# Kernel optimization log

Hardware: AMD Instinct MI355X
Metric: run time of the kernel (lower is better)

The kernel has to match this reference:

```python
import jax, jax.numpy as jnp
import numpy as np
from jax import lax

V, D, M, H, NC, S = 100000, 512, 512, 256, 5, 1024


def setup_inputs() -> dict:
    key = jax.random.key(0)
    ks = jax.random.split(key, 16)
    s = 0.05
    emb = jax.random.normal(ks[0], (V, D), jnp.float32) * s
    emb = emb.at[0].set(0.0)  # padding_idx = 0
    inp = {
        "l_ids": jax.random.randint(ks[1], (S,), 0, V),
        "r_ids": jax.random.randint(ks[2], (S,), 0, V),
        "emb": emb,
        "Wioux": jax.random.normal(ks[3], (3 * M, D), jnp.float32) * s,
        "bioux": jnp.zeros((3 * M,), jnp.float32),
        "Wiouh": jax.random.normal(ks[4], (3 * M, M), jnp.float32) * s,
        "biouh": jnp.zeros((3 * M,), jnp.float32),
        "Wfx": jax.random.normal(ks[5], (M, D), jnp.float32) * s,
        "bfx": jnp.zeros((M,), jnp.float32),
        "Wfh": jax.random.normal(ks[6], (M, M), jnp.float32) * s,
        "bfh": jnp.zeros((M,), jnp.float32),
        "Wh": jax.random.normal(ks[7], (H, 4 * M), jnp.float32) * s,
        "bh": jnp.zeros((H,), jnp.float32),
        "Wp": jax.random.normal(ks[8], (NC, H), jnp.float32) * s,
        "bp": jnp.zeros((NC,), jnp.float32),
    }
    return inp


def reference(l_ids, r_ids, emb, Wioux, bioux, Wiouh, biouh, Wfx, bfx, Wfh, bfh, Wh, bh, Wp, bp):
    def cell(x, c, h):
        # i, o, u gates fused into one [3M] GEMV pair, as in the original ioux/iouh Linears
        iou = Wioux @ x + bioux + Wiouh @ h + biouh
        i, o, u = jnp.split(iou, 3)
        f = jax.nn.sigmoid(Wfx @ x + bfx + Wfh @ h + bfh)
        # torch.sum(f*c, dim=0) over a [1, M] tensor is identity -> c' = i*u + f*c
        c2 = jax.nn.sigmoid(i) * jnp.tanh(u) + f * c
        h2 = jax.nn.sigmoid(o) * jnp.tanh(c2)
        return c2, h2

    def encode(xs):  # xs: [S, D]
        z = jnp.zeros((M,), xs.dtype)
        (_, hF), _ = lax.scan(lambda ch, x: (cell(x, ch[0], ch[1]), None), (z, z), xs)
        # 'backward' direction in the original keeps only hiddn_state_mat[0]:
        # a single cell step on the LAST token from zero state.
        _, hB = cell(xs[-1], z, z)
        return jnp.concatenate([hF, hB])  # [2M]

    lvec = encode(emb[l_ids])
    rvec = encode(emb[r_ids])
    vec = jnp.concatenate([lvec * rvec, jnp.abs(lvec - rvec)])  # [4M]
    logits = Wp @ jax.nn.sigmoid(Wh @ vec + bh) + bp
    return jax.nn.log_softmax(logits)[None, :]  # [1, NC]
```

## Files before the change

kernel.cpp:

```cpp
#include <hip/hip_runtime.h>
#include <math.h>

#define SEQLEN 1024
#define DIM 512
#define MM 512

typedef float f32x4 __attribute__((ext_vector_type(4)));
typedef float f32x2 __attribute__((ext_vector_type(2)));

__device__ __forceinline__ float sigf(float x) {
  return __builtin_amdgcn_rcpf(1.0f + __expf(-x));
}
__device__ __forceinline__ float tanhfast(float x) {
  return 1.0f - 2.0f * __builtin_amdgcn_rcpf(1.0f + __expf(2.0f * x));
}

__global__ __launch_bounds__(256) void gx_gemm(
    const int* __restrict__ l_ids, const int* __restrict__ r_ids,
    const float* __restrict__ emb,
    const float* __restrict__ Wioux, const float* __restrict__ Wfx,
    const float* __restrict__ bioux, const float* __restrict__ biouh,
    const float* __restrict__ bfx, const float* __restrict__ bfh,
    float* __restrict__ gx)
{
  __shared__ __align__(16) float At[32][68];
  __shared__ __align__(16) float Bt[32][68];
  const int tid = threadIdx.x;
  const int bid = blockIdx.x;
  const int seq = bid >> 9;
  const int tt  = (bid >> 5) & 15;
  const int gt  = bid & 31;
  const int t0 = tt * 64, g0 = gt * 64;
  const int* ids = seq ? r_ids : l_ids;

  const int li = tid >> 2;
  const int lk = (tid & 3) * 8;
  const float* arow = emb + (size_t)ids[t0 + li] * DIM;
  const int gg = g0 + li;
  const float* brow = (gg < 1536) ? (Wioux + (size_t)gg * DIM)
                                  : (Wfx + (size_t)(gg - 1536) * DIM);
  const int tr = tid >> 4;
  const int tc = tid & 15;

  float acc[4][4];
  #pragma unroll
  for (int i = 0; i < 4; ++i) { acc[i][0]=0.f; acc[i][1]=0.f; acc[i][2]=0.f; acc[i][3]=0.f; }

  for (int kb = 0; kb < 16; ++kb) {
    const int k0 = kb * 32;
    float4 av0 = *(const float4*)(arow + k0 + lk);
    float4 av1 = *(const float4*)(arow + k0 + lk + 4);
    float4 bv0 = *(const float4*)(brow + k0 + lk);
    float4 bv1 = *(const float4*)(brow + k0 + lk + 4);
    __syncthreads();
    At[lk+0][li]=av0.x; At[lk+1][li]=av0.y; At[lk+2][li]=av0.z; At[lk+3][li]=av0.w;
    At[lk+4][li]=av1.x; At[lk+5][li]=av1.y; At[lk+6][li]=av1.z; At[lk+7][li]=av1.w;
    Bt[lk+0][li]=bv0.x; Bt[lk+1][li]=bv0.y; Bt[lk+2][li]=bv0.z; Bt[lk+3][li]=bv0.w;
    Bt[lk+4][li]=bv1.x; Bt[lk+5][li]=bv1.y; Bt[lk+6][li]=bv1.z; Bt[lk+7][li]=bv1.w;
    __syncthreads();
    #pragma unroll
    for (int k = 0; k < 32; ++k) {
      float4 a4 = *(const float4*)&At[k][tr*4];
      float4 b4 = *(const float4*)&Bt[k][tc*4];
      acc[0][0]+=a4.x*b4.x; acc[0][1]+=a4.x*b4.y; acc[0][2]+=a4.x*b4.z; acc[0][3]+=a4.x*b4.w;
      acc[1][0]+=a4.y*b4.x; acc[1][1]+=a4.y*b4.y; acc[1][2]+=a4.y*b4.z; acc[1][3]+=a4.y*b4.w;
      acc[2][0]+=a4.z*b4.x; acc[2][1]+=a4.z*b4.y; acc[2][2]+=a4.z*b4.z; acc[2][3]+=a4.z*b4.w;
      acc[3][0]+=a4.w*b4.x; acc[3][1]+=a4.w*b4.y; acc[3][2]+=a4.w*b4.z; acc[3][3]+=a4.w*b4.w;
    }
  }
  const int gc = g0 + tc * 4;
  float badd[4];
  #pragma unroll
  for (int jj = 0; jj < 4; ++jj) {
    int g = gc + jj;
    badd[jj] = (g < 1536) ? (bioux[g] + biouh[g]) : (bfx[g-1536] + bfh[g-1536]);
  }
  #pragma unroll
  for (int ii = 0; ii < 4; ++ii) {
    float4 r;
    r.x = acc[ii][0] + badd[0];
    r.y = acc[ii][1] + badd[1];
    r.z = acc[ii][2] + badd[2];
    r.w = acc[ii][3] + badd[3];
    size_t off = ((size_t)seq * SEQLEN + (size_t)(t0 + tr*4 + ii)) * 2048 + gc;
    *(float4*)(gx + off) = r;
  }
}

__global__ __launch_bounds__(512, 1) void lstm_scan(
    const float* __restrict__ Wiouh, const float* __restrict__ Wfh,
    const float* __restrict__ gx,
    float* __restrict__ hbuf,
    float* __restrict__ hB)
{
  const int tid = threadIdx.x;
  const int wg  = blockIdx.x;
  const int b   = tid & 15;
  const int g   = (tid >> 4) & 1;
  const int jl  = tid >> 5;
  const int j   = wg * 16 + jl;
  const bool owner = ((tid & 31) == 0);

  const int gA = 2 * g, gB = 2 * g + 1;
  const float* rA = ((gA < 3) ? (Wiouh + ((size_t)(gA * 512 + j)) * MM)
                              : (Wfh + (size_t)j * MM)) + b * 32;
  const float* rB = ((gB < 3) ? (Wiouh + ((size_t)(gB * 512 + j)) * MM)
                              : (Wfh + (size_t)j * MM)) + b * 32;
  f32x4 wa0 = *(const f32x4*)(rA + 0),  wa1 = *(const f32x4*)(rA + 4);
  f32x4 wa2 = *(const f32x4*)(rA + 8),  wa3 = *(const f32x4*)(rA + 12);
  f32x4 wa4 = *(const f32x4*)(rA + 16), wa5 = *(const f32x4*)(rA + 20);
  f32x4 wa6 = *(const f32x4*)(rA + 24), wa7 = *(const f32x4*)(rA + 28);
  f32x4 wb0 = *(const f32x4*)(rB + 0),  wb1 = *(const f32x4*)(rB + 4);
  f32x4 wb2 = *(const f32x4*)(rB + 8),  wb3 = *(const f32x4*)(rB + 12);
  f32x4 wb4 = *(const f32x4*)(rB + 16), wb5 = *(const f32x4*)(rB + 20);
  f32x4 wb6 = *(const f32x4*)(rB + 24), wb7 = *(const f32x4*)(rB + 28);
  asm volatile("" : "+v"(wa0), "+v"(wa1), "+v"(wa2), "+v"(wa3),
                    "+v"(wa4), "+v"(wa5), "+v"(wa6), "+v"(wa7));
  asm volatile("" : "+v"(wb0), "+v"(wb1), "+v"(wb2), "+v"(wb3),
                    "+v"(wb4), "+v"(wb5), "+v"(wb6), "+v"(wb7));

  __shared__ __align__(16) float hs[2][16 * 68];

  float cl = 0.0f, cr = 0.0f;
  const float* gxs = gx;

  for (int t = 0; t < SEQLEN; ++t) {
    const float* pp = hbuf + (size_t)((t & 1) * 512 + tid) * 4;
    const float tf = (float)t;
    f32x4 eA, eB, e;
    asm volatile("global_load_dwordx4 %0, %2, off sc0 sc1\n\t"
                 "global_load_dwordx4 %1, %2, off sc0 sc1"
                 : "=&v"(eA), "=&v"(eB) : "v"(pp) : "memory");
    for (;;) {
      asm volatile("s_waitcnt vmcnt(1)" ::: "memory");
      __builtin_amdgcn_sched_barrier(0);
      if (eA[1] >= tf && eA[3] >= tf) { e = eA; break; }
      asm volatile("global_load_dwordx4 %0, %1, off sc0 sc1" : "=&v"(eA) : "v"(pp) : "memory");
      asm volatile("s_waitcnt vmcnt(1)" ::: "memory");
      __builtin_amdgcn_sched_barrier(0);
      if (eB[1] >= tf && eB[3] >= tf) { e = eB; break; }
      asm volatile("global_load_dwordx4 %0, %1, off sc0 sc1" : "=&v"(eB) : "v"(pp) : "memory");
    }
    asm volatile("s_waitcnt vmcnt(0)" ::: "memory");
    __builtin_amdgcn_sched_barrier(0);

    float gl0=0.f, gl1=0.f, gl2=0.f, gl3=0.f, gr0=0.f, gr1=0.f, gr2=0.f, gr3=0.f;
    if (owner) {
      const float* gpl = gxs + (size_t)t * 2048 + j;
      const float* gpr = gxs + ((size_t)SEQLEN + t) * 2048 + j;
      gl0 = gpl[0]; gl1 = gpl[512]; gl2 = gpl[1024]; gl3 = gpl[1536];
      gr0 = gpr[0]; gr1 = gpr[512]; gr2 = gpr[1024]; gr3 = gpr[1536];
    }

    {
      f32x2 s2; s2[0] = e[0]; s2[1] = e[2];
      *(f32x2*)&hs[t & 1][(tid >> 5) * 68 + (tid & 31) * 2] = s2;
    }
    __syncthreads();

    const float* rb = &hs[t & 1][b * 68];
    float a0l = 0.f, a0r = 0.f, a1l = 0.f, a1r = 0.f;
    #define STEPQ(q, WA, WB) { \
      f32x4 v0 = *(const f32x4*)(rb + (q)*8); \
      f32x4 v1 = *(const f32x4*)(rb + (q)*8 + 4); \
      a0l += WA[0]*v0[0]; a0r += WA[0]*v0[1]; \
      a1l += WB[0]*v0[0]; a1r += WB[0]*v0[1]; \
      a0l += WA[1]*v0[2]; a0r += WA[1]*v0[3]; \
      a1l += WB[1]*v0[2]; a1r += WB[1]*v0[3]; \
      a0l += WA[2]*v1[0]; a0r += WA[2]*v1[1]; \
      a1l += WB[2]*v1[0]; a1r += WB[2]*v1[1]; \
      a0l += WA[3]*v1[2]; a0r += WA[3]*v1[3]; \
      a1l += WB[3]*v1[2]; a1r += WB[3]*v1[3]; \
    }
    STEPQ(0, wa0, wb0) STEPQ(1, wa1, wb1) STEPQ(2, wa2, wb2) STEPQ(3, wa3, wb3)
    STEPQ(4, wa4, wb4) STEPQ(5, wa5, wb5) STEPQ(6, wa6, wb6) STEPQ(7, wa7, wb7)
    #undef STEPQ

    #pragma unroll
    for (int m = 1; m < 16; m <<= 1) {
      a0l += __shfl_xor(a0l, m, 64);
      a1l += __shfl_xor(a1l, m, 64);
      a0r += __shfl_xor(a0r, m, 64);
      a1r += __shfl_xor(a1r, m, 64);
    }
    const float p0l = __shfl_xor(a0l, 16, 64);
    const float p1l = __shfl_xor(a1l, 16, 64);
    const float p0r = __shfl_xor(a0r, 16, 64);
    const float p1r = __shfl_xor(a1r, 16, 64);

    if (owner) {
      const float il = a0l + gl0, ol = a1l + gl1, ul = p0l + gl2, fl = p1l + gl3;
      const float ir = a0r + gr0, orr = a1r + gr1, ur = p0r + gr2, fr = p1r + gr3;
      cl = sigf(il) * tanhfast(ul) + sigf(fl) * cl;
      cr = sigf(ir) * tanhfast(ur) + sigf(fr) * cr;
      const float h2l = sigf(ol) * tanhfast(cl);
      const float h2r = sigf(orr) * tanhfast(cr);
      const float tg = (float)(t + 1);
      f32x4 st; st[0] = h2l; st[1] = tg; st[2] = h2r; st[3] = tg;
      float* dp = hbuf + (size_t)((((t + 1) & 1) * 512 + j)) * 4;
      asm volatile("global_store_dwordx4 %0, %1, off sc0 sc1" :: "v"(dp), "v"(st) : "memory");
      if (t == SEQLEN - 1) {
        const float cBl = sigf(gl0) * tanhfast(gl2);
        const float cBr = sigf(gr0) * tanhfast(gr2);
        hB[j]       = sigf(gl1) * tanhfast(cBl);
        hB[512 + j] = sigf(gr1) * tanhfast(cBr);
      }
    }
  }
}

__global__ __launch_bounds__(256) void head1(
    const float* __restrict__ hbuf, const float* __restrict__ hB,
    const float* __restrict__ Wh, const float* __restrict__ bh,
    float* __restrict__ sv)
{
  __shared__ __align__(16) float vec[2048];
  const int tid = threadIdx.x;
  const int wg = blockIdx.x;
  for (int k = tid; k < 1024; k += 256) {
    float lv, rv;
    if (k < 512) { lv = hbuf[(size_t)k * 4]; rv = hbuf[(size_t)k * 4 + 2]; }
    else         { lv = hB[k - 512];         rv = hB[512 + (k - 512)]; }
    vec[k] = lv * rv;
    vec[1024 + k] = fabsf(lv - rv);
  }
  __syncthreads();
  const int row = wg * 16 + (tid >> 4);
  const int ln = tid & 15;
  const float* wr = Wh + (size_t)row * 2048 + ln * 128;
  const float* vp = vec + ln * 128;
  float acc = 0.0f;
  #pragma unroll
  for (int k = 0; k < 128; k += 4) {
    float4 wv = *(const float4*)(wr + k);
    float4 vv = *(const float4*)(vp + k);
    acc += wv.x*vv.x + wv.y*vv.y + wv.z*vv.z + wv.w*vv.w;
  }
  #pragma unroll
  for (int msk = 1; msk < 16; msk <<= 1) acc += __shfl_xor(acc, msk, 64);
  if (ln == 0) sv[row] = 1.0f / (1.0f + expf(-(acc + bh[row])));
}

__global__ __launch_bounds__(256) void head2(
    const float* __restrict__ sv, const float* __restrict__ Wp,
    const float* __restrict__ bp, float* __restrict__ out)
{
  __shared__ float s_l[256];
  __shared__ float lg[5];
  const int tid = threadIdx.x;
  s_l[tid] = sv[tid];
  __syncthreads();
  if (tid < 5) {
    float acc = bp[tid];
    for (int k = 0; k < 256; ++k) acc += Wp[tid*256 + k] * s_l[k];
    lg[tid] = acc;
  }
  __syncthreads();
  if (tid == 0) {
    float mx = lg[0];
    #pragma unroll
    for (int i = 1; i < 5; ++i) mx = fmaxf(mx, lg[i]);
    float sum = 0.0f;
    #pragma unroll
    for (int i = 0; i < 5; ++i) sum += expf(lg[i] - mx);
    const float lse = mx + logf(sum);
    #pragma unroll
    for (int i = 0; i < 5; ++i) out[i] = lg[i] - lse;
  }
}

extern "C" void kernel_launch(void* const* d_in, const int* in_sizes, int n_in,
                              void* d_out, int out_size, void* d_ws, size_t ws_size,
                              hipStream_t stream) {
  const int*   l_ids = (const int*)d_in[0];
  const int*   r_ids = (const int*)d_in[1];
  const float* emb   = (const float*)d_in[2];
  const float* Wioux = (const float*)d_in[3];
  const float* bioux = (const float*)d_in[4];
  const float* Wiouh = (const float*)d_in[5];
  const float* biouh = (const float*)d_in[6];
  const float* Wfx   = (const float*)d_in[7];
  const float* bfx   = (const float*)d_in[8];
  const float* Wfh   = (const float*)d_in[9];
  const float* bfh   = (const float*)d_in[10];
  const float* Wh    = (const float*)d_in[11];
  const float* bh    = (const float*)d_in[12];
  const float* Wp    = (const float*)d_in[13];
  const float* bp    = (const float*)d_in[14];
  float* out = (float*)d_out;

  float* gx   = (float*)d_ws;
  float* hbuf = gx + (size_t)2*1024*2048;
  float* hB   = hbuf + 4096;
  float* sv   = hB + 1024;

  hipMemsetAsync(hbuf, 0, (4096 + 1024 + 256) * sizeof(float), stream);

  gx_gemm<<<dim3(1024), dim3(256), 0, stream>>>(l_ids, r_ids, emb, Wioux, Wfx,
                                                bioux, biouh, bfx, bfh, gx);
  lstm_scan<<<dim3(32), dim3(512), 0, stream>>>(Wiouh, Wfh, gx, hbuf, hB);
  head1<<<dim3(16), dim3(256), 0, stream>>>(hbuf, hB, Wh, bh, sv);
  head2<<<dim3(1), dim3(256), 0, stream>>>(sv, Wp, bp, out);
  (void)in_sizes; (void)n_in; (void)out_size; (void)ws_size;
}
```

Baseline: 2.168 ms.

## Split left/right recurrences into interleaved phases with separate flag buffers

Result: slower. 3.416 ms (+57.5%).

```diff
diff --git a/kernel.cpp b/kernel.cpp
--- a/kernel.cpp
+++ b/kernel.cpp
@@ -119,94 +119,83 @@
   asm volatile("" : "+v"(wb0), "+v"(wb1), "+v"(wb2), "+v"(wb3),
                     "+v"(wb4), "+v"(wb5), "+v"(wb6), "+v"(wb7));
 
-  __shared__ __align__(16) float hs[2][16 * 68];
-
-  float cl = 0.0f, cr = 0.0f;
-  const float* gxs = gx;
+  __shared__ __align__(16) float hs[2][2][16 * 36];
+
+  float cL = 0.0f, cR = 0.0f;
+  f32x2 spL, spR;
+
+  {
+    const float* p0 = hbuf + (size_t)tid * 2;
+    const float* p1 = hbuf + (size_t)(2 * 512 + tid) * 2;
+    asm volatile("global_load_dwordx2 %0, %2, off sc0 sc1\n\t"
+                 "global_load_dwordx2 %1, %3, off sc0 sc1"
+                 : "=&v"(spL), "=&v"(spR) : "v"(p0), "v"(p1) : "memory");
+  }
+
+  #define PHASE(SP, SQ, CVAR, T) do {                                          \
+    const int par = (T) & 1;                                                   \
+    float* hb = hbuf + (size_t)((SQ) * 2 + par) * 1024;                        \
+    const float tf = (float)(T);                                               \
+       \
+    asm volatile("s_waitcnt vmcnt(0)" ::: "memory");                           \
+    __builtin_amdgcn_sched_barrier(0);                                         \
+    asm volatile("" : "+v"(SP));                                               \
+    f32x2 e = SP;                                                              \
+    const float* pp = hb + (size_t)tid * 2;                                    \
+    for (;;) {                                                                 \
+      if (e[1] >= tf) break;                                                   \
+      asm volatile("global_load_dwordx2 %0, %1, off sc0 sc1\n\t"               \
+                   "s_waitcnt vmcnt(0)" : "=&v"(e) : "v"(pp) : "memory");      \
+    }                                                                          \
+                   \
+    float g0v=0.f, g1v=0.f, g2v=0.f, g3v=0.f;                                  \
+    if (owner) {                                                               \
+      const float* gp = gx + ((size_t)(SQ) * SEQLEN + (T)) * 2048 + j;         \
+      g0v = gp[0]; g1v = gp[512]; g2v = gp[1024]; g3v = gp[1536];              \
+    }                                                                          \
+                                                   \
+    hs[SQ][par][(tid >> 5) * 36 + (tid & 31)] = e[0];                          \
+    __syncthreads();                                                           \
+                                                    \
+    const float* rb = &hs[SQ][par][b * 36];                                    \
+    f32x4 h0 = *(const f32x4*)(rb + 0),  h1 = *(const f32x4*)(rb + 4);         \
+    f32x4 h2 = *(const f32x4*)(rb + 8),  h3 = *(const f32x4*)(rb + 12);        \
+    f32x4 h4 = *(const f32x4*)(rb + 16), h5 = *(const f32x4*)(rb + 20);        \
+    f32x4 h6 = *(const f32x4*)(rb + 24), h7 = *(const f32x4*)(rb + 28);        \
+    f32x4 v0 = wa0*h0; v0 += wa1*h1; v0 += wa2*h2; v0 += wa3*h3;               \
+    v0 += wa4*h4; v0 += wa5*h5; v0 += wa6*h6; v0 += wa7*h7;                    \
+    f32x4 v1 = wb0*h0; v1 += wb1*h1; v1 += wb2*h2; v1 += wb3*h3;               \
+    v1 += wb4*h4; v1 += wb5*h5; v1 += wb6*h6; v1 += wb7*h7;                    \
+    float a0 = v0[0] + v0[1] + v0[2] + v0[3];                                  \
+    float a1 = v1[0] + v1[1] + v1[2] + v1[3];                                  \
+    a0 += __shfl_xor(a0, 1, 64);  a1 += __shfl_xor(a1, 1, 64);                 \
+    a0 += __shfl_xor(a0, 2, 64);  a1 += __shfl_xor(a1, 2, 64);                 \
+    a0 += __shfl_xor(a0, 4, 64);  a1 += __shfl_xor(a1, 4, 64);                 \
+    a0 += __shfl_xor(a0, 8, 64);  a1 += __shfl_xor(a1, 8, 64);                 \
+    const float p0 = __shfl_xor(a0, 16, 64);                                   \
+    const float p1 = __shfl_xor(a1, 16, 64);                                   \
+    if (owner) {                                                               \
+      const float iv = a0 + g0v, ov = a1 + g1v, uv = p0 + g2v, fv = p1 + g3v;  \
+      CVAR = sigf(iv) * tanhfast(uv) + sigf(fv) * CVAR;                        \
+      const float h2o = sigf(ov) * tanhfast(CVAR);                             \
+      f32x2 st; st[0] = h2o; st[1] = (float)((T) + 1);                         \
+      float* dp = hbuf + (size_t)((SQ) * 2 + (((T) + 1) & 1)) * 1024 + (size_t)j * 2; \
+      asm volatile("global_store_dwordx2 %0, %1, off sc0 sc1" :: "v"(dp), "v"(st) : "memory"); \
+      if ((T) == SEQLEN - 1) {                                                 \
+        const float cB = sigf(g0v) * tanhfast(g2v);                            \
+        hB[(SQ) * 512 + j] = sigf(g1v) * tanhfast(cB);                         \
+      }                                                                        \
+    }                                                                          \
+     \
+    const float* ppn = hbuf + (size_t)((SQ) * 2 + (((T) + 1) & 1)) * 1024 + (size_t)tid * 2; \
+    asm volatile("global_load_dwordx2 %0, %1, off sc0 sc1" : "=&v"(SP) : "v"(ppn) : "memory"); \
+  } while (0)
 
   for (int t = 0; t < SEQLEN; ++t) {
-    const float* pp = hbuf + (size_t)((t & 1) * 512 + tid) * 4;
-    const float tf = (float)t;
-    f32x4 eA, eB, e;
-    asm volatile("global_load_dwordx4 %0, %2, off sc0 sc1\n\t"
-                 "global_load_dwordx4 %1, %2, off sc0 sc1"
-                 : "=&v"(eA), "=&v"(eB) : "v"(pp) : "memory");
-    for (;;) {
-      asm volatile("s_waitcnt vmcnt(1)" ::: "memory");
-      __builtin_amdgcn_sched_barrier(0);
-      if (eA[1] >= tf && eA[3] >= tf) { e = eA; break; }
-      asm volatile("global_load_dwordx4 %0, %1, off sc0 sc1" : "=&v"(eA) : "v"(pp) : "memory");
-      asm volatile("s_waitcnt vmcnt(1)" ::: "memory");
-      __builtin_amdgcn_sched_barrier(0);
-      if (eB[1] >= tf && eB[3] >= tf) { e = eB; break; }
-      asm volatile("global_load_dwordx4 %0, %1, off sc0 sc1" : "=&v"(eB) : "v"(pp) : "memory");
-    }
-    asm volatile("s_waitcnt vmcnt(0)" ::: "memory");
-    __builtin_amdgcn_sched_barrier(0);
-
-    float gl0=0.f, gl1=0.f, gl2=0.f, gl3=0.f, gr0=0.f, gr1=0.f, gr2=0.f, gr3=0.f;
-    if (owner) {
-      const float* gpl = gxs + (size_t)t * 2048 + j;
-      const float* gpr = gxs + ((size_t)SEQLEN + t) * 2048 + j;
-      gl0 = gpl[0]; gl1 = gpl[512]; gl2 = gpl[1024]; gl3 = gpl[1536];
-      gr0 = gpr[0]; gr1 = gpr[512]; gr2 = gpr[1024]; gr3 = gpr[1536];
-    }
-
-    {
-      f32x2 s2; s2[0] = e[0]; s2[1] = e[2];
-      *(f32x2*)&hs[t & 1][(tid >> 5) * 68 + (tid & 31) * 2] = s2;
-    }
-    __syncthreads();
-
-    const float* rb = &hs[t & 1][b * 68];
-    float a0l = 0.f, a0r = 0.f, a1l = 0.f, a1r = 0.f;
-    #define STEPQ(q, WA, WB) { \
-      f32x4 v0 = *(const f32x4*)(rb + (q)*8); \
-      f32x4 v1 = *(const f32x4*)(rb + (q)*8 + 4); \
-      a0l += WA[0]*v0[0]; a0r += WA[0]*v0[1]; \
-      a1l += WB[0]*v0[0]; a1r += WB[0]*v0[1]; \
-      a0l += WA[1]*v0[2]; a0r += WA[1]*v0[3]; \
-      a1l += WB[1]*v0[2]; a1r += WB[1]*v0[3]; \
-      a0l += WA[2]*v1[0]; a0r += WA[2]*v1[1]; \
-      a1l += WB[2]*v1[0]; a1r += WB[2]*v1[1]; \
-      a0l += WA[3]*v1[2]; a0r += WA[3]*v1[3]; \
-      a1l += WB[3]*v1[2]; a1r += WB[3]*v1[3]; \
-    }
-    STEPQ(0, wa0, wb0) STEPQ(1, wa1, wb1) STEPQ(2, wa2, wb2) STEPQ(3, wa3, wb3)
-    STEPQ(4, wa4, wb4) STEPQ(5, wa5, wb5) STEPQ(6, wa6, wb6) STEPQ(7, wa7, wb7)
-    #undef STEPQ
-
-    #pragma unroll
-    for (int m = 1; m < 16; m <<= 1) {
-      a0l += __shfl_xor(a0l, m, 64);
-      a1l += __shfl_xor(a1l, m, 64);
-      a0r += __shfl_xor(a0r, m, 64);
-      a1r += __shfl_xor(a1r, m, 64);
-    }
-    const float p0l = __shfl_xor(a0l, 16, 64);
-    const float p1l = __shfl_xor(a1l, 16, 64);
-    const float p0r = __shfl_xor(a0r, 16, 64);
-    const float p1r = __shfl_xor(a1r, 16, 64);
-
-    if (owner) {
-      const float il = a0l + gl0, ol = a1l + gl1, ul = p0l + gl2, fl = p1l + gl3;
-      const float ir = a0r + gr0, orr = a1r + gr1, ur = p0r + gr2, fr = p1r + gr3;
-      cl = sigf(il) * tanhfast(ul) + sigf(fl) * cl;
-      cr = sigf(ir) * tanhfast(ur) + sigf(fr) * cr;
-      const float h2l = sigf(ol) * tanhfast(cl);
-      const float h2r = sigf(orr) * tanhfast(cr);
-      const float tg = (float)(t + 1);
-      f32x4 st; st[0] = h2l; st[1] = tg; st[2] = h2r; st[3] = tg;
-      float* dp = hbuf + (size_t)((((t + 1) & 1) * 512 + j)) * 4;
-      asm volatile("global_store_dwordx4 %0, %1, off sc0 sc1" :: "v"(dp), "v"(st) : "memory");
-      if (t == SEQLEN - 1) {
-        const float cBl = sigf(gl0) * tanhfast(gl2);
-        const float cBr = sigf(gr0) * tanhfast(gr2);
-        hB[j]       = sigf(gl1) * tanhfast(cBl);
-        hB[512 + j] = sigf(gr1) * tanhfast(cBr);
-      }
-    }
-  }
+    PHASE(spL, 0, cL, t);
+    PHASE(spR, 1, cR, t);
+  }
+  #undef PHASE
 }
 
 __global__ __launch_bounds__(256) void head1(
@@ -219,7 +208,7 @@
   const int wg = blockIdx.x;
   for (int k = tid; k < 1024; k += 256) {
     float lv, rv;
-    if (k < 512) { lv = hbuf[(size_t)k * 4]; rv = hbuf[(size_t)k * 4 + 2]; }
+    if (k < 512) { lv = hbuf[(size_t)k * 2]; rv = hbuf[2048 + (size_t)k * 2]; }
     else         { lv = hB[k - 512];         rv = hB[512 + (k - 512)]; }
     vec[k] = lv * rv;
     vec[1024 + k] = fabsf(lv - rv);
```

## Prefetch input-gate projections into double-buffered LDS in 16-step chunks

Applied to the files above, without the earlier changes.

After: 2.908 ms. 34.1% more time.

```diff
diff --git a/kernel.cpp b/kernel.cpp
--- a/kernel.cpp
+++ b/kernel.cpp
@@ -120,9 +120,29 @@
                     "+v"(wb4), "+v"(wb5), "+v"(wb6), "+v"(wb7));
 
   __shared__ __align__(16) float hs[2][16 * 68];
+  __shared__ __align__(16) float gw[2][2048];
+
+  const int rf_seq  = tid >> 8;
+  const int rf_tq   = (tid >> 6) & 3;
+  const int rf_gate = (tid >> 4) & 3;
+  const int rf_jl   = tid & 15;
+  const float* rf_base = gx + (size_t)rf_seq * SEQLEN * 2048
+                            + (size_t)rf_gate * 512 + wg * 16 + rf_jl;
+  const int rf_lds = rf_seq * 1024 + rf_tq * 256 + rf_gate * 16 + rf_jl;
+
+  {
+    const float* p = rf_base + (size_t)(rf_tq * 4) * 2048;
+    const float v0 = p[0];
+    const float v1 = p[2048];
+    const float v2 = p[4096];
+    const float v3 = p[6144];
+    gw[0][rf_lds + 0]   = v0;
+    gw[0][rf_lds + 64]  = v1;
+    gw[0][rf_lds + 128] = v2;
+    gw[0][rf_lds + 192] = v3;
+  }
 
   float cl = 0.0f, cr = 0.0f;
-  const float* gxs = gx;
 
   for (int t = 0; t < SEQLEN; ++t) {
     const float* pp = hbuf + (size_t)((t & 1) * 512 + tid) * 4;
@@ -144,12 +164,14 @@
     asm volatile("s_waitcnt vmcnt(0)" ::: "memory");
     __builtin_amdgcn_sched_barrier(0);
 
-    float gl0=0.f, gl1=0.f, gl2=0.f, gl3=0.f, gr0=0.f, gr1=0.f, gr2=0.f, gr3=0.f;
-    if (owner) {
-      const float* gpl = gxs + (size_t)t * 2048 + j;
-      const float* gpr = gxs + ((size_t)SEQLEN + t) * 2048 + j;
-      gl0 = gpl[0]; gl1 = gpl[512]; gl2 = gpl[1024]; gl3 = gpl[1536];
-      gr0 = gpr[0]; gr1 = gpr[512]; gr2 = gpr[1024]; gr3 = gpr[1536];
+    float rv0 = 0.f, rv1 = 0.f, rv2 = 0.f, rv3 = 0.f;
+    const bool refill = ((t & 15) == 15) && (t != SEQLEN - 1);
+    if (refill) {
+      const float* p = rf_base + (size_t)(t + 1 + rf_tq * 4) * 2048;
+      rv0 = p[0];
+      rv1 = p[2048];
+      rv2 = p[4096];
+      rv3 = p[6144];
     }
 
     {
@@ -157,6 +179,13 @@
       *(f32x2*)&hs[t & 1][(tid >> 5) * 68 + (tid & 31) * 2] = s2;
     }
     __syncthreads();
+
+    float gl0=0.f, gl1=0.f, gl2=0.f, gl3=0.f, gr0=0.f, gr1=0.f, gr2=0.f, gr3=0.f;
+    if (owner) {
+      const float* gp = &gw[(t >> 4) & 1][(t & 15) * 64 + jl];
+      gl0 = gp[0];    gl1 = gp[16];     gl2 = gp[32];     gl3 = gp[48];
+      gr0 = gp[1024]; gr1 = gp[1040];   gr2 = gp[1056];   gr3 = gp[1072];
+    }
 
     const float* rb = &hs[t & 1][b * 68];
     float a0l = 0.f, a0r = 0.f, a1l = 0.f, a1r = 0.f;
@@ -205,6 +234,14 @@
         hB[j]       = sigf(gl1) * tanhfast(cBl);
         hB[512 + j] = sigf(gr1) * tanhfast(cBr);
       }
+    }
+
+    if (refill) {
+      const int nb = ((t >> 4) + 1) & 1;
+      gw[nb][rf_lds + 0]   = rv0;
+      gw[nb][rf_lds + 64]  = rv1;
+      gw[nb][rf_lds + 128] = rv2;
+      gw[nb][rf_lds + 192] = rv3;
     }
   }
 }
```
